# Kernel optimization log

Hardware: AMD Instinct MI355X
Metric: run time of the kernel (lower is better)

Reference implementation:

```python
import jax, jax.numpy as jnp
import numpy as np
from jax import lax

DIM = 192
HEADS = 4
HIDDEN = int(DIM * 2.66)  # 510
B, H, W = 2, 64, 64
EPS_LN = 1e-6
EPS_NORM = 1e-12


def conv1x1(x, w, b):
    # x: (b,c,h,w), w: (o,c), b: (o,)
    return jnp.einsum('bchw,oc->bohw', x, w) + b[None, :, None, None]


def dwconv3x3(x, w, b):
    # depthwise 3x3, SAME padding; w: (C,1,3,3)
    c = x.shape[1]
    y = lax.conv_general_dilated(x, w, window_strides=(1, 1), padding='SAME',
                                 feature_group_count=c,
                                 dimension_numbers=('NCHW', 'OIHW', 'NCHW'))
    return y + b[None, :, None, None]


def layernorm2d(x, w, b):
    mean = jnp.mean(x, axis=(2, 3), keepdims=True)
    var = jnp.mean((x - mean) ** 2, axis=(2, 3), keepdims=True)
    return (x - mean) / jnp.sqrt(var + EPS_LN) * w[None, :, None, None] + b[None, :, None, None]


def mdta(x, qkv_w, qkv_b, qkv_dw_w, qkv_dw_b, temperature, proj_w, proj_b):
    b, c, h, w = x.shape
    qkv = dwconv3x3(conv1x1(x, qkv_w, qkv_b), qkv_dw_w, qkv_dw_b)
    q, k, v = jnp.split(qkv, 3, axis=1)
    dh = c // HEADS
    q = q.reshape(b, HEADS, dh, h * w)
    k = k.reshape(b, HEADS, dh, h * w)
    v = v.reshape(b, HEADS, dh, h * w)
    # L2-normalize over per-head channel dim (axis=2), like F.normalize(dim=2)
    q = q / jnp.maximum(jnp.linalg.norm(q, axis=2, keepdims=True), EPS_NORM)
    k = k / jnp.maximum(jnp.linalg.norm(k, axis=2, keepdims=True), EPS_NORM)
    # spatial attention map: (b, heads, HW, HW)
    attn = jnp.einsum('bhcn,bhcm->bhnm', q, k) * temperature[None]  # temp (heads,1,1)
    attn = jax.nn.softmax(attn, axis=-1)
    out = jnp.einsum('bhnm,bhcm->bhcn', attn, v)  # (b,heads,dh,HW)
    out = out.reshape(b, c, h, w)
    return conv1x1(out, proj_w, proj_b)


def gdfn(x, pin_w, pin_b, dw_w, dw_b, pout_w, pout_b):
    y = dwconv3x3(conv1x1(x, pin_w, pin_b), dw_w, dw_b)
    y1, y2 = jnp.split(y, 2, axis=1)
    y = jax.nn.gelu(y1, approximate=False) * y2
    return conv1x1(y, pout_w, pout_b)


def setup_inputs() -> dict:
    key = jax.random.key(0)
    ks = jax.random.split(key, 8)
    s = 0.02
    return {
        'x': jax.random.normal(ks[0], (B, DIM, H, W), jnp.float32),
        'ln1_w': jnp.ones((DIM,), jnp.float32),
        'ln1_b': jnp.zeros((DIM,), jnp.float32),
        'qkv_w': jax.random.normal(ks[1], (DIM * 3, DIM), jnp.float32) * s,
        'qkv_b': jnp.zeros((DIM * 3,), jnp.float32),
        'qkv_dw_w': jax.random.normal(ks[2], (DIM * 3, 1, 3, 3), jnp.float32) * s,
        'qkv_dw_b': jnp.zeros((DIM * 3,), jnp.float32),
        'temperature': jnp.ones((HEADS, 1, 1), jnp.float32),
        'proj_w': jax.random.normal(ks[3], (DIM, DIM), jnp.float32) * s,
        'proj_b': jnp.zeros((DIM,), jnp.float32),
        'ln2_w': jnp.ones((DIM,), jnp.float32),
        'ln2_b': jnp.zeros((DIM,), jnp.float32),
        'pin_w': jax.random.normal(ks[4], (HIDDEN * 2, DIM), jnp.float32) * s,
        'pin_b': jnp.zeros((HIDDEN * 2,), jnp.float32),
        'gdfn_dw_w': jax.random.normal(ks[5], (HIDDEN * 2, 1, 3, 3), jnp.float32) * s,
        'gdfn_dw_b': jnp.zeros((HIDDEN * 2,), jnp.float32),
        'pout_w': jax.random.normal(ks[6], (DIM, HIDDEN), jnp.float32) * s,
        'pout_b': jnp.zeros((DIM,), jnp.float32),
    }


def reference(x, ln1_w, ln1_b, qkv_w, qkv_b, qkv_dw_w, qkv_dw_b, temperature,
              proj_w, proj_b, ln2_w, ln2_b, pin_w, pin_b, gdfn_dw_w, gdfn_dw_b,
              pout_w, pout_b):
    x = x + mdta(layernorm2d(x, ln1_w, ln1_b), qkv_w, qkv_b, qkv_dw_w, qkv_dw_b,
                 temperature, proj_w, proj_b)
    x = x + gdfn(layernorm2d(x, ln2_w, ln2_b), pin_w, pin_b, gdfn_dw_w, gdfn_dw_b,
                 pout_w, pout_b)
    return x
```

## Files before the change

kernel.cpp:

```cpp
#include <hip/hip_runtime.h>
#include <hip/hip_bf16.h>

typedef __bf16 bf16x8 __attribute__((ext_vector_type(8)));
typedef __bf16 bf16x4 __attribute__((ext_vector_type(4)));
typedef __bf16 bf16x2 __attribute__((ext_vector_type(2)));
typedef float f32x4 __attribute__((ext_vector_type(4)));

#define HW 4096
#define DIMC 192
#define DH 48
#define HIDC 510

__global__ void wcvt4_kernel(const float* __restrict__ qkv_w, const float* __restrict__ proj_w,
                             const float* __restrict__ pin_w, const float* __restrict__ pout_w,
                             __bf16* __restrict__ wb_qkv, __bf16* __restrict__ wb_proj,
                             __bf16* __restrict__ wb_pin, __bf16* __restrict__ wb_pout) {
  int idx = blockIdx.x * 256 + threadIdx.x;
  if (idx < 110592) {
    wb_qkv[idx] = (__bf16)qkv_w[idx];
  } else if (idx < 147456) {
    int i = idx - 110592;
    wb_proj[i] = (__bf16)proj_w[i];
  } else if (idx < 343296) {
    int i = idx - 147456;
    wb_pin[i] = (__bf16)pin_w[i];
  } else if (idx < 441600) {
    int i = idx - 343296;
    int o = i >> 9, c = i & 511;
    wb_pout[i] = (c < HIDC) ? (__bf16)pout_w[o * HIDC + c] : (__bf16)0.f;
  }
}

__global__ __launch_bounds__(256) void ln_stats_kernel(const float* __restrict__ x, const float* __restrict__ w,
                                                       const float* __restrict__ b, float* __restrict__ sc,
                                                       float* __restrict__ sh) {
  int bc = blockIdx.x;
  int c = bc % DIMC;
  const float* row = x + (size_t)bc * HW;
  float s = 0.f, s2 = 0.f;
  for (int i = threadIdx.x; i < HW; i += 256) { float v = row[i]; s += v; s2 = fmaf(v, v, s2); }
  __shared__ float red[8];
  for (int off = 32; off; off >>= 1) { s += __shfl_down(s, off, 64); s2 += __shfl_down(s2, off, 64); }
  int wid = threadIdx.x >> 6;
  if ((threadIdx.x & 63) == 0) { red[wid] = s; red[4 + wid] = s2; }
  __syncthreads();
  if (threadIdx.x == 0) {
    s = red[0] + red[1] + red[2] + red[3];
    s2 = red[4] + red[5] + red[6] + red[7];
    float mean = s * (1.f / HW);
    float var = s2 * (1.f / HW) - mean * mean;
    float rstd = rsqrtf(var + 1e-6f);
    float scv = rstd * w[c];
    sc[bc] = scv;
    sh[bc] = b[c] - mean * scv;
  }
}

__global__ __launch_bounds__(256) void ln_apply_t_kernel(const float* __restrict__ x, const float* __restrict__ sc,
                                                         const float* __restrict__ sh, __bf16* __restrict__ Xt) {
  int n0 = blockIdx.x * 64, c0 = blockIdx.y * 32, b = blockIdx.z;
  int t = threadIdx.x;
  int n = t & 63, cs = c0 + (t >> 6) * 8;
  __bf16 ob[8];
#pragma unroll
  for (int cc = 0; cc < 8; ++cc) {
    int c = cs + cc;
    float v = fmaf(x[((size_t)(b * DIMC + c)) * HW + n0 + n], sc[b * DIMC + c], sh[b * DIMC + c]);
    ob[cc] = (__bf16)v;
  }
  *(bf16x8*)&Xt[((size_t)((b << 12) + n0 + n)) * DIMC + cs] = *(bf16x8*)ob;
}

__global__ __launch_bounds__(256) void gemm_kernel(const __bf16* __restrict__ A, const __bf16* __restrict__ Bt,
                                                   const float* __restrict__ bias, const float* __restrict__ res,
                                                   float* __restrict__ outf, __bf16* __restrict__ outb,
                                                   int O, int Cs, int mode) {
  __shared__ __align__(16) __bf16 Asub[64 * 72];
  __shared__ __align__(16) __bf16 Bsub[128 * 72];
  const int t = threadIdx.x;
  const int lane = t & 63, wv = t >> 6;
  const int q4 = lane >> 4, l16 = lane & 15;
  int o0 = blockIdx.y * 64;
  if (o0 + 64 > O) o0 = O - 64;
  const int ntot0 = blockIdx.x * 128;
  const int b = ntot0 >> 12;
  const int n_in_b0 = ntot0 & 4095;

  f32x4 acc[8];
#pragma unroll
  for (int nt = 0; nt < 8; ++nt) acc[nt] = (f32x4){0.f, 0.f, 0.f, 0.f};

  for (int c0 = 0; c0 < Cs; c0 += 64) {
    __syncthreads();
#pragma unroll
    for (int j = 0; j < 2; ++j) {
      int id = t + 256 * j;
      *(bf16x8*)&Asub[(id >> 3) * 72 + (id & 7) * 8] =
          *(const bf16x8*)&A[((size_t)(o0 + (id >> 3))) * Cs + c0 + (id & 7) * 8];
    }
    if (mode != 3) {
#pragma unroll
      for (int j = 0; j < 4; ++j) {
        int id = t + 256 * j;
        *(bf16x8*)&Bsub[(id >> 3) * 72 + (id & 7) * 8] =
            *(const bf16x8*)&Bt[((size_t)(ntot0 + (id >> 3))) * Cs + c0 + (id & 7) * 8];
      }
    } else {
      int cr = t >> 2, seg = t & 3;
      int cg = c0 + cr;
      __bf16 tmp[32];
      if (cg < HIDC) {
        const __bf16* gp = Bt + ((size_t)(b * HIDC + cg)) * HW + n_in_b0 + seg * 32;
#pragma unroll
        for (int j = 0; j < 4; ++j) *(bf16x8*)&tmp[8 * j] = *(const bf16x8*)&gp[8 * j];
      } else {
#pragma unroll
        for (int k = 0; k < 32; ++k) tmp[k] = (__bf16)0.f;
      }
#pragma unroll
      for (int k = 0; k < 32; ++k) Bsub[(seg * 32 + k) * 72 + cr] = tmp[k];
    }
    __syncthreads();
#pragma unroll
    for (int ks = 0; ks < 2; ++ks) {
      bf16x8 af = *(const bf16x8*)&Asub[(16 * wv + l16) * 72 + 32 * ks + 8 * q4];
#pragma unroll
      for (int nt = 0; nt < 8; ++nt) {
        bf16x8 bfr = *(const bf16x8*)&Bsub[(16 * nt + l16) * 72 + 32 * ks + 8 * q4];
        acc[nt] = __builtin_amdgcn_mfma_f32_16x16x32_bf16(af, bfr, acc[nt], 0, 0, 0);
      }
    }
  }

  float bvals[4];
#pragma unroll
  for (int r = 0; r < 4; ++r) bvals[r] = bias[o0 + 16 * wv + 4 * q4 + r];
#pragma unroll
  for (int nt = 0; nt < 8; ++nt) {
    int n_in_b = n_in_b0 + 16 * nt + l16;
#pragma unroll
    for (int r = 0; r < 4; ++r) {
      int o = o0 + 16 * wv + 4 * q4 + r;
      size_t addr = ((size_t)(b * O + o)) * HW + n_in_b;
      float v = acc[nt][r] + bvals[r];
      if (mode >= 2) { outf[addr] = v + res[addr]; }
      else if (mode == 0) { outf[addr] = v; }
      else { outb[addr] = (__bf16)v; }
    }
  }
}

__global__ __launch_bounds__(256) void dwconv_split_kernel(const __bf16* __restrict__ in, const float* __restrict__ w,
                                                           const float* __restrict__ bias,
                                                           __bf16* __restrict__ qdwb, __bf16* __restrict__ Vbf) {
  int bc = blockIdx.x;
  int b = bc / 576, ch = bc - b * 576;
  __shared__ float tile[66 * 68];
  for (int i = threadIdx.x; i < 66 * 68; i += 256) tile[i] = 0.f;
  __syncthreads();
  const __bf16* p = in + (size_t)bc * HW;
  for (int j = 0; j < 8; ++j) {
    int i = 2 * threadIdx.x + 512 * j;
    bf16x2 v = *(const bf16x2*)&p[i];
    int y = i >> 6, xx = i & 63;
    tile[(y + 1) * 68 + xx + 1] = (float)v.x;
    tile[(y + 1) * 68 + xx + 2] = (float)v.y;
  }
  __syncthreads();
  float w0 = w[ch * 9 + 0], w1 = w[ch * 9 + 1], w2 = w[ch * 9 + 2];
  float w3 = w[ch * 9 + 3], w4 = w[ch * 9 + 4], w5 = w[ch * 9 + 5];
  float w6 = w[ch * 9 + 6], w7 = w[ch * 9 + 7], w8 = w[ch * 9 + 8];
  float bb = bias[ch];
  __bf16* dst;
  if (ch < 384) dst = qdwb + ((size_t)(b * 384 + ch)) * HW;
  else {
    int c = ch - 384, h = c / DH, cc = c - h * DH;
    dst = Vbf + ((size_t)((b * 4 + h) * DH + cc)) * HW;
  }
  for (int j = 0; j < 8; ++j) {
    int i = 2 * threadIdx.x + 512 * j;
    int y = i >> 6, xx = i & 63;
    const float* tt = &tile[y * 68 + xx];
    float a = bb;
    a = fmaf(w0, tt[0], a);   a = fmaf(w1, tt[1], a);   a = fmaf(w2, tt[2], a);
    a = fmaf(w3, tt[68], a);  a = fmaf(w4, tt[69], a);  a = fmaf(w5, tt[70], a);
    a = fmaf(w6, tt[136], a); a = fmaf(w7, tt[137], a); a = fmaf(w8, tt[138], a);
    float a2 = bb;
    a2 = fmaf(w0, tt[1], a2);   a2 = fmaf(w1, tt[2], a2);   a2 = fmaf(w2, tt[3], a2);
    a2 = fmaf(w3, tt[69], a2);  a2 = fmaf(w4, tt[70], a2);  a2 = fmaf(w5, tt[71], a2);
    a2 = fmaf(w6, tt[137], a2); a2 = fmaf(w7, tt[138], a2); a2 = fmaf(w8, tt[139], a2);
    bf16x2 o = { (__bf16)a, (__bf16)a2 };
    *(bf16x2*)&dst[i] = o;
  }
}

__global__ __launch_bounds__(256) void gdfn_dw_gate_kernel(const __bf16* __restrict__ hid, const float* __restrict__ w,
                                                           const float* __restrict__ bias, __bf16* __restrict__ gate) {
  int blk = blockIdx.x;
  int b = blk / HIDC, j = blk - b * HIDC;
  __shared__ float t1[66 * 68];
  __shared__ float t2[66 * 68];
  for (int i = threadIdx.x; i < 66 * 68; i += 256) { t1[i] = 0.f; t2[i] = 0.f; }
  __syncthreads();
  const __bf16* p1 = hid + ((size_t)b * (2 * HIDC) + j) * HW;
  const __bf16* p2 = p1 + (size_t)HIDC * HW;
  for (int i = threadIdx.x; i < HW; i += 256) {
    int y = i >> 6, xx = i & 63;
    t1[(y + 1) * 68 + xx + 1] = (float)p1[i];
    t2[(y + 1) * 68 + xx + 1] = (float)p2[i];
  }
  __syncthreads();
  int c1 = j, c2 = j + HIDC;
  float a0 = w[c1*9+0], a1w = w[c1*9+1], a2w = w[c1*9+2], a3 = w[c1*9+3], a4 = w[c1*9+4],
        a5 = w[c1*9+5], a6 = w[c1*9+6], a7 = w[c1*9+7], a8 = w[c1*9+8];
  float b0 = w[c2*9+0], b1 = w[c2*9+1], b2 = w[c2*9+2], b3 = w[c2*9+3], b4 = w[c2*9+4],
        b5 = w[c2*9+5], b6 = w[c2*9+6], b7 = w[c2*9+7], b8 = w[c2*9+8];
  float bi1 = bias[c1], bi2 = bias[c2];
  __bf16* op = gate + ((size_t)b * HIDC + j) * HW;
  for (int i = threadIdx.x; i < HW; i += 256) {
    int y = i >> 6, xx = i & 63;
    const float* u = &t1[y * 68 + xx];
    const float* v = &t2[y * 68 + xx];
    float x1 = bi1;
    x1 = fmaf(a0, u[0], x1);   x1 = fmaf(a1w, u[1], x1);  x1 = fmaf(a2w, u[2], x1);
    x1 = fmaf(a3, u[68], x1);  x1 = fmaf(a4, u[69], x1);  x1 = fmaf(a5, u[70], x1);
    x1 = fmaf(a6, u[136], x1); x1 = fmaf(a7, u[137], x1); x1 = fmaf(a8, u[138], x1);
    float x2 = bi2;
    x2 = fmaf(b0, v[0], x2);   x2 = fmaf(b1, v[1], x2);   x2 = fmaf(b2, v[2], x2);
    x2 = fmaf(b3, v[68], x2);  x2 = fmaf(b4, v[69], x2);  x2 = fmaf(b5, v[70], x2);
    x2 = fmaf(b6, v[136], x2); x2 = fmaf(b7, v[137], x2); x2 = fmaf(b8, v[138], x2);
    float g = 0.5f * x1 * (1.f + erff(x1 * 0.70710678118654752f));
    op[i] = (__bf16)(g * x2);
  }
}

__global__ __launch_bounds__(256) void prep_qk_kernel(const __bf16* __restrict__ qdwb, const float* __restrict__ temp,
                                                      __bf16* __restrict__ Qbf, __bf16* __restrict__ Kbf) {
  int gid = blockIdx.x * 256 + threadIdx.x;
  int bh = gid >> 12, n = gid & 4095;
  int b = bh >> 2, h = bh & 3;
  const __bf16* qp = qdwb + ((size_t)(b * 384 + h * DH)) * HW + n;
  const __bf16* kp = qp + (size_t)192 * HW;
  float buf[DH];
  float ss = 0.f;
#pragma unroll
  for (int c = 0; c < DH; ++c) { buf[c] = (float)qp[(size_t)c * HW]; ss = fmaf(buf[c], buf[c], ss); }
  float sc = temp[h] / fmaxf(sqrtf(ss), 1e-12f);
  __bf16 ob[64];
#pragma unroll
  for (int c = 0; c < DH; ++c) ob[c] = (__bf16)(buf[c] * sc);
#pragma unroll
  for (int c = DH; c < 64; ++c) ob[c] = (__bf16)0.f;
  __bf16* qd = Qbf + (size_t)gid * 64;
#pragma unroll
  for (int ch = 0; ch < 8; ++ch) *(bf16x8*)&qd[ch * 8] = *(bf16x8*)&ob[ch * 8];

  ss = 0.f;
#pragma unroll
  for (int c = 0; c < DH; ++c) { buf[c] = (float)kp[(size_t)c * HW]; ss = fmaf(buf[c], buf[c], ss); }
  sc = 1.f / fmaxf(sqrtf(ss), 1e-12f);
#pragma unroll
  for (int c = 0; c < DH; ++c) ob[c] = (__bf16)(buf[c] * sc);
  __bf16* kd = Kbf + (size_t)gid * 64;
#pragma unroll
  for (int ch = 0; ch < 8; ++ch) *(bf16x8*)&kd[ch * 8] = *(bf16x8*)&ob[ch * 8];
}

__global__ __launch_bounds__(256) void attn_split_kernel(const __bf16* __restrict__ Qbf, const __bf16* __restrict__ Kbf,
                                                         const __bf16* __restrict__ Vbf, float* __restrict__ part) {
  __shared__ __align__(16) __bf16 Kt[64 * 72];
  __shared__ __align__(16) __bf16 Vc[48 * 72];
  __shared__ __align__(16) __bf16 Pl[64 * 72];
  const int tid = threadIdx.x;
  const int lane = tid & 63;
  const int wv = tid >> 6;
  const int q4 = lane >> 4, l16 = lane & 15;
  const int bid = blockIdx.x;
  const int chunk = bid >> 9, rest = bid & 511;
  const int bh = rest >> 6, nt = rest & 63;
  const int n0 = nt * 64;
  const __bf16* Qg = Qbf + (size_t)bh * HW * 64;
  const __bf16* Kg = Kbf + (size_t)bh * HW * 64;
  const __bf16* Vg = Vbf + (size_t)bh * DH * HW;

  bf16x8 qf[4][2];
#pragma unroll
  for (int s = 0; s < 4; ++s)
#pragma unroll
    for (int ks = 0; ks < 2; ++ks)
      qf[s][ks] = *(const bf16x8*)&Qg[((size_t)(n0 + 16 * s + l16)) * 64 + 32 * ks + 8 * q4];

  float lsub[4] = {0.f, 0.f, 0.f, 0.f};
  f32x4 oacc[3];
#pragma unroll
  for (int ct = 0; ct < 3; ++ct) oacc[ct] = (f32x4){0.f, 0.f, 0.f, 0.f};

  for (int mt = chunk * 16; mt < chunk * 16 + 16; ++mt) {
    const int m0 = mt * 64;
    __syncthreads();
#pragma unroll
    for (int j = 0; j < 2; ++j) {
      int id = tid + 256 * j;
      *(bf16x8*)&Kt[(id >> 3) * 72 + (id & 7) * 8] = *(const bf16x8*)&Kg[((size_t)(m0 + (id >> 3))) * 64 + (id & 7) * 8];
    }
    for (int i = tid; i < 384; i += 256)
      *(bf16x8*)&Vc[(i >> 3) * 72 + (i & 7) * 8] = *(const bf16x8*)&Vg[((size_t)(i >> 3)) * HW + m0 + (i & 7) * 8];
    __syncthreads();

    f32x4 sacc[4];
#pragma unroll
    for (int s = 0; s < 4; ++s) sacc[s] = (f32x4){0.f, 0.f, 0.f, 0.f};
#pragma unroll
    for (int ks = 0; ks < 2; ++ks) {
      bf16x8 af = *(const bf16x8*)&Kt[(16 * wv + l16) * 72 + 32 * ks + 8 * q4];
#pragma unroll
      for (int s = 0; s < 4; ++s)
        sacc[s] = __builtin_amdgcn_mfma_f32_16x16x32_bf16(af, qf[s][ks], sacc[s], 0, 0, 0);
    }

#pragma unroll
    for (int s = 0; s < 4; ++s) {
      float p0 = __expf(sacc[s][0]);
      float p1 = __expf(sacc[s][1]);
      float p2 = __expf(sacc[s][2]);
      float p3 = __expf(sacc[s][3]);
      lsub[s] += (p0 + p1) + (p2 + p3);
      bf16x4 pk = { (__bf16)p0, (__bf16)p1, (__bf16)p2, (__bf16)p3 };
      *(bf16x4*)&Pl[(16 * s + l16) * 72 + 16 * wv + 4 * q4] = pk;
    }
    __syncthreads();

#pragma unroll
    for (int ks = 0; ks < 2; ++ks) {
      bf16x8 pf = *(const bf16x8*)&Pl[(16 * wv + l16) * 72 + 32 * ks + 8 * q4];
#pragma unroll
      for (int ct = 0; ct < 3; ++ct) {
        bf16x8 vf = *(const bf16x8*)&Vc[(16 * ct + l16) * 72 + 32 * ks + 8 * q4];
        oacc[ct] = __builtin_amdgcn_mfma_f32_16x16x32_bf16(pf, vf, oacc[ct], 0, 0, 0);
      }
    }
  }

  __syncthreads();
  float* Lred = (float*)Kt;
#pragma unroll
  for (int s = 0; s < 4; ++s) {
    float v = lsub[s];
    v += __shfl_xor(v, 16, 64);
    v += __shfl_xor(v, 32, 64);
    if (q4 == 0) Lred[wv * 64 + 16 * s + l16] = v;
  }
  __syncthreads();
  size_t pbase = (size_t)bid * 3136;
  if (tid < 64)
    part[pbase + 3072 + tid] = Lred[tid] + Lred[64 + tid] + Lred[128 + tid] + Lred[192 + tid];
#pragma unroll
  for (int ct = 0; ct < 3; ++ct)
#pragma unroll
    for (int r = 0; r < 4; ++r) {
      int n = 16 * wv + 4 * q4 + r;
      part[pbase + (size_t)n * 48 + 16 * ct + l16] = oacc[ct][r];
    }
}

__global__ __launch_bounds__(256) void attn_merge_kernel(const float* __restrict__ part, __bf16* __restrict__ Xt) {
  const int bid = blockIdx.x;
  const int bh = bid >> 6, nt = bid & 63;
  const int b = bh >> 2, h = bh & 3;
  const int n0 = nt * 64;
  const int t = threadIdx.x;
  __shared__ float linv[64];
  if (t < 64) {
    float s = 0.f;
#pragma unroll
    for (int ch = 0; ch < 4; ++ch) s += part[((size_t)(ch * 512 + bid)) * 3136 + 3072 + t];
    linv[t] = 1.f / s;
  }
  __syncthreads();
#pragma unroll
  for (int j = 0; j < 3; ++j) {
    int id = t + 256 * j;
    int n = id / 12, cc = (id - n * 12) * 4;
    f32x4 s = (f32x4){0.f, 0.f, 0.f, 0.f};
#pragma unroll
    for (int ch = 0; ch < 4; ++ch) s += *(const f32x4*)&part[((size_t)(ch * 512 + bid)) * 3136 + (size_t)n * 48 + cc];
    float li = linv[n];
    bf16x4 ov = { (__bf16)(s.x * li), (__bf16)(s.y * li), (__bf16)(s.z * li), (__bf16)(s.w * li) };
    *(bf16x4*)&Xt[((size_t)((b << 12) + n0 + n)) * DIMC + h * DH + cc] = ov;
  }
}

extern "C" void kernel_launch(void* const* d_in, const int* in_sizes, int n_in,
                              void* d_out, int out_size, void* d_ws, size_t ws_size,
                              hipStream_t stream) {
  const float* x        = (const float*)d_in[0];
  const float* ln1_w    = (const float*)d_in[1];
  const float* ln1_b    = (const float*)d_in[2];
  const float* qkv_w    = (const float*)d_in[3];
  const float* qkv_b    = (const float*)d_in[4];
  const float* qkv_dw_w = (const float*)d_in[5];
  const float* qkv_dw_b = (const float*)d_in[6];
  const float* temperature = (const float*)d_in[7];
  const float* proj_w   = (const float*)d_in[8];
  const float* proj_b   = (const float*)d_in[9];
  const float* ln2_w    = (const float*)d_in[10];
  const float* ln2_b    = (const float*)d_in[11];
  const float* pin_w    = (const float*)d_in[12];
  const float* pin_b    = (const float*)d_in[13];
  const float* gdfn_dw_w = (const float*)d_in[14];
  const float* gdfn_dw_b = (const float*)d_in[15];
  const float* pout_w   = (const float*)d_in[16];
  const float* pout_b   = (const float*)d_in[17];
  float* out = (float*)d_out;
  float* ws = (float*)d_ws;

  __bf16* wb_qkv  = (__bf16*)(ws + 0);
  __bf16* wb_proj = (__bf16*)(ws + 55296);
  __bf16* wb_pin  = (__bf16*)(ws + 73728);
  __bf16* wb_pout = (__bf16*)(ws + 171648);
  float* sc1 = ws + 220800;
  float* sh1 = ws + 221184;
  float* sc2 = ws + 221568;
  float* sh2 = ws + 221952;
  __bf16* Xt1 = (__bf16*)(ws + 222336);
  __bf16* Xt2 = (__bf16*)(ws + 222336);
  __bf16* Qbf = (__bf16*)(ws + 222336);
  __bf16* Kbf = (__bf16*)(ws + 1270912);
  __bf16* Vbf = (__bf16*)(ws + 2319488);
  __bf16* qkvb   = (__bf16*)(ws + 3105920);
  __bf16* Xt_att = (__bf16*)(ws + 3105920);
  __bf16* hid    = (__bf16*)(ws + 3105920);
  __bf16* qdwb  = (__bf16*)(ws + 5465216);
  float*  Opart = ws + 5465216;
  __bf16* gate  = (__bf16*)(ws + 7283840);

  wcvt4_kernel<<<1725, 256, 0, stream>>>(qkv_w, proj_w, pin_w, pout_w, wb_qkv, wb_proj, wb_pin, wb_pout);

  ln_stats_kernel<<<2 * DIMC, 256, 0, stream>>>(x, ln1_w, ln1_b, sc1, sh1);
  ln_apply_t_kernel<<<dim3(64, 6, 2), 256, 0, stream>>>(x, sc1, sh1, Xt1);
  gemm_kernel<<<dim3(64, 9), 256, 0, stream>>>(wb_qkv, Xt1, qkv_b, nullptr, nullptr, qkvb, 576, 192, 1);
  dwconv_split_kernel<<<1152, 256, 0, stream>>>(qkvb, qkv_dw_w, qkv_dw_b, qdwb, Vbf);
  prep_qk_kernel<<<128, 256, 0, stream>>>(qdwb, temperature, Qbf, Kbf);
  attn_split_kernel<<<2048, 256, 0, stream>>>(Qbf, Kbf, Vbf, Opart);
  attn_merge_kernel<<<512, 256, 0, stream>>>(Opart, Xt_att);
  gemm_kernel<<<dim3(64, 3), 256, 0, stream>>>(wb_proj, Xt_att, proj_b, x, out, nullptr, 192, 192, 2);

  ln_stats_kernel<<<2 * DIMC, 256, 0, stream>>>(out, ln2_w, ln2_b, sc2, sh2);
  ln_apply_t_kernel<<<dim3(64, 6, 2), 256, 0, stream>>>(out, sc2, sh2, Xt2);
  gemm_kernel<<<dim3(64, 16), 256, 0, stream>>>(wb_pin, Xt2, pin_b, nullptr, nullptr, hid, 1020, 192, 1);
  gdfn_dw_gate_kernel<<<2 * HIDC, 256, 0, stream>>>(hid, gdfn_dw_w, gdfn_dw_b, gate);
  gemm_kernel<<<dim3(64, 3), 256, 0, stream>>>(wb_pout, (const __bf16*)gate, pout_b, out, out, nullptr, 192, 512, 3);
}
```

Baseline: 268.9 us.

## Feed softmax probabilities straight from registers into fp16 PV MFMA

The P tile no longer round-trips through shared memory. The exponentiated scores are packed to fp16 in registers and used directly as the B operand of a 16x16x16 f16 MFMA, with V stored as fp16 so the layouts match. Each wave now holds partial O for all 64 query rows over its own 16 keys, so a cross-wave shared-memory reduction is added at the end. Q is prescaled by log2(e) so exp2f can replace __expf, and launch bounds request 4 blocks per SM. The trade is one fewer barrier and less LDS traffic per key tile, against more accumulator registers (48 floats) and an extra reduction epilogue.

```diff
diff --git a/kernel.cpp b/kernel.cpp
--- a/kernel.cpp
+++ b/kernel.cpp
@@ -4,12 +4,18 @@
 typedef __bf16 bf16x8 __attribute__((ext_vector_type(8)));
 typedef __bf16 bf16x4 __attribute__((ext_vector_type(4)));
 typedef __bf16 bf16x2 __attribute__((ext_vector_type(2)));
+typedef _Float16 f16x8 __attribute__((ext_vector_type(8)));
+typedef _Float16 f16x4 __attribute__((ext_vector_type(4)));
+typedef _Float16 f16x2 __attribute__((ext_vector_type(2)));
 typedef float f32x4 __attribute__((ext_vector_type(4)));
+
+#define MFMA16x16x16F16(a, b, c) __builtin_amdgcn_mfma_f32_16x16x16f16((a), (b), (c), 0, 0, 0)
 
 #define HW 4096
 #define DIMC 192
 #define DH 48
 #define HIDC 510
+#define LOG2E 1.44269504088896f
 
 __global__ void wcvt4_kernel(const float* __restrict__ qkv_w, const float* __restrict__ proj_w,
                              const float* __restrict__ pin_w, const float* __restrict__ pout_w,
@@ -152,7 +158,7 @@
 
 __global__ __launch_bounds__(256) void dwconv_split_kernel(const __bf16* __restrict__ in, const float* __restrict__ w,
                                                            const float* __restrict__ bias,
-                                                           __bf16* __restrict__ qdwb, __bf16* __restrict__ Vbf) {
+                                                           __bf16* __restrict__ qdwb, _Float16* __restrict__ Vh) {
   int bc = blockIdx.x;
   int b = bc / 576, ch = bc - b * 576;
   __shared__ float tile[66 * 68];
@@ -171,11 +177,12 @@
   float w3 = w[ch * 9 + 3], w4 = w[ch * 9 + 4], w5 = w[ch * 9 + 5];
   float w6 = w[ch * 9 + 6], w7 = w[ch * 9 + 7], w8 = w[ch * 9 + 8];
   float bb = bias[ch];
-  __bf16* dst;
-  if (ch < 384) dst = qdwb + ((size_t)(b * 384 + ch)) * HW;
+  const bool isv = (ch >= 384);
+  __bf16* dstq = nullptr; _Float16* dstv = nullptr;
+  if (!isv) dstq = qdwb + ((size_t)(b * 384 + ch)) * HW;
   else {
     int c = ch - 384, h = c / DH, cc = c - h * DH;
-    dst = Vbf + ((size_t)((b * 4 + h) * DH + cc)) * HW;
+    dstv = Vh + ((size_t)((b * 4 + h) * DH + cc)) * HW;
   }
   for (int j = 0; j < 8; ++j) {
     int i = 2 * threadIdx.x + 512 * j;
@@ -189,8 +196,13 @@
     a2 = fmaf(w0, tt[1], a2);   a2 = fmaf(w1, tt[2], a2);   a2 = fmaf(w2, tt[3], a2);
     a2 = fmaf(w3, tt[69], a2);  a2 = fmaf(w4, tt[70], a2);  a2 = fmaf(w5, tt[71], a2);
     a2 = fmaf(w6, tt[137], a2); a2 = fmaf(w7, tt[138], a2); a2 = fmaf(w8, tt[139], a2);
-    bf16x2 o = { (__bf16)a, (__bf16)a2 };
-    *(bf16x2*)&dst[i] = o;
+    if (!isv) {
+      bf16x2 o = { (__bf16)a, (__bf16)a2 };
+      *(bf16x2*)&dstq[i] = o;
+    } else {
+      f16x2 o = { (_Float16)a, (_Float16)a2 };
+      *(f16x2*)&dstv[i] = o;
+    }
   }
 }
 
@@ -245,7 +257,7 @@
   float ss = 0.f;
 #pragma unroll
   for (int c = 0; c < DH; ++c) { buf[c] = (float)qp[(size_t)c * HW]; ss = fmaf(buf[c], buf[c], ss); }
-  float sc = temp[h] / fmaxf(sqrtf(ss), 1e-12f);
+  float sc = temp[h] * LOG2E / fmaxf(sqrtf(ss), 1e-12f);
   __bf16 ob[64];
 #pragma unroll
   for (int c = 0; c < DH; ++c) ob[c] = (__bf16)(buf[c] * sc);
@@ -266,11 +278,12 @@
   for (int ch = 0; ch < 8; ++ch) *(bf16x8*)&kd[ch * 8] = *(bf16x8*)&ob[ch * 8];
 }
 
-__global__ __launch_bounds__(256) void attn_split_kernel(const __bf16* __restrict__ Qbf, const __bf16* __restrict__ Kbf,
-                                                         const __bf16* __restrict__ Vbf, float* __restrict__ part) {
-  __shared__ __align__(16) __bf16 Kt[64 * 72];
-  __shared__ __align__(16) __bf16 Vc[48 * 72];
-  __shared__ __align__(16) __bf16 Pl[64 * 72];
+__global__ __launch_bounds__(256, 4) void attn_split_kernel(const __bf16* __restrict__ Qbf, const __bf16* __restrict__ Kbf,
+                                                            const _Float16* __restrict__ Vh, float* __restrict__ part) {
+  __shared__ __align__(16) char smem[16384];
+  __bf16* Kt = (__bf16*)smem;
+  _Float16* Vc = (_Float16*)(smem + 9216);
+  float* sred = (float*)smem;
   const int tid = threadIdx.x;
   const int lane = tid & 63;
   const int wv = tid >> 6;
@@ -281,7 +294,7 @@
   const int n0 = nt * 64;
   const __bf16* Qg = Qbf + (size_t)bh * HW * 64;
   const __bf16* Kg = Kbf + (size_t)bh * HW * 64;
-  const __bf16* Vg = Vbf + (size_t)bh * DH * HW;
+  const _Float16* Vg = Vh + (size_t)bh * DH * HW;
 
   bf16x8 qf[4][2];
 #pragma unroll
@@ -291,9 +304,11 @@
       qf[s][ks] = *(const bf16x8*)&Qg[((size_t)(n0 + 16 * s + l16)) * 64 + 32 * ks + 8 * q4];
 
   float lsub[4] = {0.f, 0.f, 0.f, 0.f};
-  f32x4 oacc[3];
-#pragma unroll
-  for (int ct = 0; ct < 3; ++ct) oacc[ct] = (f32x4){0.f, 0.f, 0.f, 0.f};
+  f32x4 oacc[4][3];
+#pragma unroll
+  for (int s = 0; s < 4; ++s)
+#pragma unroll
+    for (int ct = 0; ct < 3; ++ct) oacc[s][ct] = (f32x4){0.f, 0.f, 0.f, 0.f};
 
   for (int mt = chunk * 16; mt < chunk * 16 + 16; ++mt) {
     const int m0 = mt * 64;
@@ -304,8 +319,13 @@
       *(bf16x8*)&Kt[(id >> 3) * 72 + (id & 7) * 8] = *(const bf16x8*)&Kg[((size_t)(m0 + (id >> 3))) * 64 + (id & 7) * 8];
     }
     for (int i = tid; i < 384; i += 256)
-      *(bf16x8*)&Vc[(i >> 3) * 72 + (i & 7) * 8] = *(const bf16x8*)&Vg[((size_t)(i >> 3)) * HW + m0 + (i & 7) * 8];
+      *(f16x8*)&Vc[(i >> 3) * 72 + (i & 7) * 8] = *(const f16x8*)&Vg[((size_t)(i >> 3)) * HW + m0 + (i & 7) * 8];
     __syncthreads();
+
+    f16x4 va[3];
+#pragma unroll
+    for (int ct = 0; ct < 3; ++ct)
+      va[ct] = *(const f16x4*)&Vc[(16 * ct + l16) * 72 + 16 * wv + 4 * q4];
 
     f32x4 sacc[4];
 #pragma unroll
@@ -320,47 +340,57 @@
 
 #pragma unroll
     for (int s = 0; s < 4; ++s) {
-      float p0 = __expf(sacc[s][0]);
-      float p1 = __expf(sacc[s][1]);
-      float p2 = __expf(sacc[s][2]);
-      float p3 = __expf(sacc[s][3]);
+      float p0 = exp2f(sacc[s][0]);
+      float p1 = exp2f(sacc[s][1]);
+      float p2 = exp2f(sacc[s][2]);
+      float p3 = exp2f(sacc[s][3]);
       lsub[s] += (p0 + p1) + (p2 + p3);
-      bf16x4 pk = { (__bf16)p0, (__bf16)p1, (__bf16)p2, (__bf16)p3 };
-      *(bf16x4*)&Pl[(16 * s + l16) * 72 + 16 * wv + 4 * q4] = pk;
-    }
-    __syncthreads();
-
-#pragma unroll
-    for (int ks = 0; ks < 2; ++ks) {
-      bf16x8 pf = *(const bf16x8*)&Pl[(16 * wv + l16) * 72 + 32 * ks + 8 * q4];
-#pragma unroll
-      for (int ct = 0; ct < 3; ++ct) {
-        bf16x8 vf = *(const bf16x8*)&Vc[(16 * ct + l16) * 72 + 32 * ks + 8 * q4];
-        oacc[ct] = __builtin_amdgcn_mfma_f32_16x16x32_bf16(pf, vf, oacc[ct], 0, 0, 0);
-      }
-    }
-  }
-
-  __syncthreads();
-  float* Lred = (float*)Kt;
+      f16x4 pk = { (_Float16)p0, (_Float16)p1, (_Float16)p2, (_Float16)p3 };
+#pragma unroll
+      for (int ct = 0; ct < 3; ++ct)
+        oacc[s][ct] = MFMA16x16x16F16(va[ct], pk, oacc[s][ct]);
+    }
+  }
+
+  __syncthreads();
+#define DUMP()  { _Pragma("unroll") for (int s = 0; s < 4; ++s) _Pragma("unroll") for (int ct = 0; ct < 3; ++ct) _Pragma("unroll") for (int r = 0; r < 4; ++r) sred[(((s * 3 + ct) * 4) + r) * 64 + (q4 << 4) + l16] = oacc[s][ct][r]; }
+#define ACCUM() { _Pragma("unroll") for (int s = 0; s < 4; ++s) _Pragma("unroll") for (int ct = 0; ct < 3; ++ct) _Pragma("unroll") for (int r = 0; r < 4; ++r) oacc[s][ct][r] += sred[(((s * 3 + ct) * 4) + r) * 64 + (q4 << 4) + l16]; }
+  if (wv == 1) DUMP();
+  __syncthreads();
+  if (wv == 0) ACCUM();
+  __syncthreads();
+  if (wv == 3) DUMP();
+  __syncthreads();
+  if (wv == 2) ACCUM();
+  __syncthreads();
+  if (wv == 2) DUMP();
+  __syncthreads();
+  if (wv == 0) ACCUM();
+  __syncthreads();
+  if (wv == 0) DUMP();
+  __syncthreads();
+  size_t pbase = (size_t)bid * 3136;
+#pragma unroll
+  for (int k2 = 0; k2 < 3; ++k2) {
+    int id = tid + 256 * k2;
+    int n = id / 12, c0 = (id - n * 12) * 4;
+    int s = n >> 4, lx = n & 15, ct = c0 >> 4, qx = (c0 >> 2) & 3;
+    f32x4 v;
+#pragma unroll
+    for (int r = 0; r < 4; ++r) v[r] = sred[((s * 3 + ct) * 4 + r) * 64 + (qx << 4) + lx];
+    *(f32x4*)&part[pbase + 4 * id] = v;
+  }
+  __syncthreads();
 #pragma unroll
   for (int s = 0; s < 4; ++s) {
     float v = lsub[s];
     v += __shfl_xor(v, 16, 64);
     v += __shfl_xor(v, 32, 64);
-    if (q4 == 0) Lred[wv * 64 + 16 * s + l16] = v;
-  }
-  __syncthreads();
-  size_t pbase = (size_t)bid * 3136;
+    if (q4 == 0) sred[wv * 64 + 16 * s + l16] = v;
+  }
+  __syncthreads();
   if (tid < 64)
-    part[pbase + 3072 + tid] = Lred[tid] + Lred[64 + tid] + Lred[128 + tid] + Lred[192 + tid];
-#pragma unroll
-  for (int ct = 0; ct < 3; ++ct)
-#pragma unroll
-    for (int r = 0; r < 4; ++r) {
-      int n = 16 * wv + 4 * q4 + r;
-      part[pbase + (size_t)n * 48 + 16 * ct + l16] = oacc[ct][r];
-    }
+    part[pbase + 3072 + tid] = sred[tid] + sred[64 + tid] + sred[128 + tid] + sred[192 + tid];
 }
 
 __global__ __launch_bounds__(256) void attn_merge_kernel(const float* __restrict__ part, __bf16* __restrict__ Xt) {
@@ -426,7 +456,7 @@
   __bf16* Xt2 = (__bf16*)(ws + 222336);
   __bf16* Qbf = (__bf16*)(ws + 222336);
   __bf16* Kbf = (__bf16*)(ws + 1270912);
-  __bf16* Vbf = (__bf16*)(ws + 2319488);
+  _Float16* Vh = (_Float16*)(ws + 2319488);
   __bf16* qkvb   = (__bf16*)(ws + 3105920);
   __bf16* Xt_att = (__bf16*)(ws + 3105920);
   __bf16* hid    = (__bf16*)(ws + 3105920);
@@ -439,9 +469,9 @@
   ln_stats_kernel<<<2 * DIMC, 256, 0, stream>>>(x, ln1_w, ln1_b, sc1, sh1);
   ln_apply_t_kernel<<<dim3(64, 6, 2), 256, 0, stream>>>(x, sc1, sh1, Xt1);
   gemm_kernel<<<dim3(64, 9), 256, 0, stream>>>(wb_qkv, Xt1, qkv_b, nullptr, nullptr, qkvb, 576, 192, 1);
-  dwconv_split_kernel<<<1152, 256, 0, stream>>>(qkvb, qkv_dw_w, qkv_dw_b, qdwb, Vbf);
+  dwconv_split_kernel<<<1152, 256, 0, stream>>>(qkvb, qkv_dw_w, qkv_dw_b, qdwb, Vh);
   prep_qk_kernel<<<128, 256, 0, stream>>>(qdwb, temperature, Qbf, Kbf);
-  attn_split_kernel<<<2048, 256, 0, stream>>>(Qbf, Kbf, Vbf, Opart);
+  attn_split_kernel<<<2048, 256, 0, stream>>>(Qbf, Kbf, Vh, Opart);
   attn_merge_kernel<<<512, 256, 0, stream>>>(Opart, Xt_att);
   gemm_kernel<<<dim3(64, 3), 256, 0, stream>>>(wb_proj, Xt_att, proj_b, x, out, nullptr, 192, 192, 2);
 
```

Result: no change. 274.1 us (+1.9%).

## Prefetch K/V tiles into registers, halve attention split, fold log2e into Q

Applied to the files above, without the earlier changes.

The attention kernel now loads the next K and V tiles into registers while the current tile is computed, so global load latency overlaps with the MFMA work. The split over keys drops from 4 chunks to 2, which halves the partial-result writes and the merge reads but also halves the number of blocks. log2(e) is folded into the Q scale so the softmax can use exp2f. The cost is extra registers per thread and lower block-level parallelism.

```diff
diff --git a/kernel.cpp b/kernel.cpp
--- a/kernel.cpp
+++ b/kernel.cpp
@@ -10,6 +10,7 @@
 #define DIMC 192
 #define DH 48
 #define HIDC 510
+#define LOG2E 1.44269504088896f
 
 __global__ void wcvt4_kernel(const float* __restrict__ qkv_w, const float* __restrict__ proj_w,
                              const float* __restrict__ pin_w, const float* __restrict__ pout_w,
@@ -245,7 +246,7 @@
   float ss = 0.f;
 #pragma unroll
   for (int c = 0; c < DH; ++c) { buf[c] = (float)qp[(size_t)c * HW]; ss = fmaf(buf[c], buf[c], ss); }
-  float sc = temp[h] / fmaxf(sqrtf(ss), 1e-12f);
+  float sc = temp[h] * LOG2E / fmaxf(sqrtf(ss), 1e-12f);
   __bf16 ob[64];
 #pragma unroll
   for (int c = 0; c < DH; ++c) ob[c] = (__bf16)(buf[c] * sc);
@@ -290,21 +291,52 @@
     for (int ks = 0; ks < 2; ++ks)
       qf[s][ks] = *(const bf16x8*)&Qg[((size_t)(n0 + 16 * s + l16)) * 64 + 32 * ks + 8 * q4];
 
+  bf16x8 kreg[2], vreg[2];
+  {
+    const int m0 = chunk * 32 * 64;
+#pragma unroll
+    for (int j = 0; j < 2; ++j) {
+      int id = tid + 256 * j;
+      kreg[j] = *(const bf16x8*)&Kg[((size_t)(m0 + (id >> 3))) * 64 + (id & 7) * 8];
+    }
+    vreg[0] = *(const bf16x8*)&Vg[((size_t)(tid >> 3)) * HW + m0 + (tid & 7) * 8];
+    if (tid < 128) {
+      int i = tid + 256;
+      vreg[1] = *(const bf16x8*)&Vg[((size_t)(i >> 3)) * HW + m0 + (i & 7) * 8];
+    }
+  }
+
   float lsub[4] = {0.f, 0.f, 0.f, 0.f};
   f32x4 oacc[3];
 #pragma unroll
   for (int ct = 0; ct < 3; ++ct) oacc[ct] = (f32x4){0.f, 0.f, 0.f, 0.f};
 
-  for (int mt = chunk * 16; mt < chunk * 16 + 16; ++mt) {
-    const int m0 = mt * 64;
+  const int mt_end = chunk * 32 + 32;
+  for (int mt = chunk * 32; mt < mt_end; ++mt) {
     __syncthreads();
 #pragma unroll
     for (int j = 0; j < 2; ++j) {
       int id = tid + 256 * j;
-      *(bf16x8*)&Kt[(id >> 3) * 72 + (id & 7) * 8] = *(const bf16x8*)&Kg[((size_t)(m0 + (id >> 3))) * 64 + (id & 7) * 8];
-    }
-    for (int i = tid; i < 384; i += 256)
-      *(bf16x8*)&Vc[(i >> 3) * 72 + (i & 7) * 8] = *(const bf16x8*)&Vg[((size_t)(i >> 3)) * HW + m0 + (i & 7) * 8];
+      *(bf16x8*)&Kt[(id >> 3) * 72 + (id & 7) * 8] = kreg[j];
+    }
+    *(bf16x8*)&Vc[(tid >> 3) * 72 + (tid & 7) * 8] = vreg[0];
+    if (tid < 128) {
+      int i = tid + 256;
+      *(bf16x8*)&Vc[(i >> 3) * 72 + (i & 7) * 8] = vreg[1];
+    }
+    if (mt + 1 < mt_end) {
+      const int m1 = (mt + 1) * 64;
+#pragma unroll
+      for (int j = 0; j < 2; ++j) {
+        int id = tid + 256 * j;
+        kreg[j] = *(const bf16x8*)&Kg[((size_t)(m1 + (id >> 3))) * 64 + (id & 7) * 8];
+      }
+      vreg[0] = *(const bf16x8*)&Vg[((size_t)(tid >> 3)) * HW + m1 + (tid & 7) * 8];
+      if (tid < 128) {
+        int i = tid + 256;
+        vreg[1] = *(const bf16x8*)&Vg[((size_t)(i >> 3)) * HW + m1 + (i & 7) * 8];
+      }
+    }
     __syncthreads();
 
     f32x4 sacc[4];
@@ -320,10 +352,10 @@
 
 #pragma unroll
     for (int s = 0; s < 4; ++s) {
-      float p0 = __expf(sacc[s][0]);
-      float p1 = __expf(sacc[s][1]);
-      float p2 = __expf(sacc[s][2]);
-      float p3 = __expf(sacc[s][3]);
+      float p0 = exp2f(sacc[s][0]);
+      float p1 = exp2f(sacc[s][1]);
+      float p2 = exp2f(sacc[s][2]);
+      float p3 = exp2f(sacc[s][3]);
       lsub[s] += (p0 + p1) + (p2 + p3);
       bf16x4 pk = { (__bf16)p0, (__bf16)p1, (__bf16)p2, (__bf16)p3 };
       *(bf16x4*)&Pl[(16 * s + l16) * 72 + 16 * wv + 4 * q4] = pk;
@@ -373,7 +405,7 @@
   if (t < 64) {
     float s = 0.f;
 #pragma unroll
-    for (int ch = 0; ch < 4; ++ch) s += part[((size_t)(ch * 512 + bid)) * 3136 + 3072 + t];
+    for (int ch = 0; ch < 2; ++ch) s += part[((size_t)(ch * 512 + bid)) * 3136 + 3072 + t];
     linv[t] = 1.f / s;
   }
   __syncthreads();
@@ -383,7 +415,7 @@
     int n = id / 12, cc = (id - n * 12) * 4;
     f32x4 s = (f32x4){0.f, 0.f, 0.f, 0.f};
 #pragma unroll
-    for (int ch = 0; ch < 4; ++ch) s += *(const f32x4*)&part[((size_t)(ch * 512 + bid)) * 3136 + (size_t)n * 48 + cc];
+    for (int ch = 0; ch < 2; ++ch) s += *(const f32x4*)&part[((size_t)(ch * 512 + bid)) * 3136 + (size_t)n * 48 + cc];
     float li = linv[n];
     bf16x4 ov = { (__bf16)(s.x * li), (__bf16)(s.y * li), (__bf16)(s.z * li), (__bf16)(s.w * li) };
     *(bf16x4*)&Xt[((size_t)((b << 12) + n0 + n)) * DIMC + h * DH + cc] = ov;
@@ -441,7 +473,7 @@
   gemm_kernel<<<dim3(64, 9), 256, 0, stream>>>(wb_qkv, Xt1, qkv_b, nullptr, nullptr, qkvb, 576, 192, 1);
   dwconv_split_kernel<<<1152, 256, 0, stream>>>(qkvb, qkv_dw_w, qkv_dw_b, qdwb, Vbf);
   prep_qk_kernel<<<128, 256, 0, stream>>>(qdwb, temperature, Qbf, Kbf);
-  attn_split_kernel<<<2048, 256, 0, stream>>>(Qbf, Kbf, Vbf, Opart);
+  attn_split_kernel<<<1024, 256, 0, stream>>>(Qbf, Kbf, Vbf, Opart);
   attn_merge_kernel<<<512, 256, 0, stream>>>(Opart, Xt_att);
   gemm_kernel<<<dim3(64, 3), 256, 0, stream>>>(wb_proj, Xt_att, proj_b, x, out, nullptr, 192, 192, 2);
 
```

Result: no change. 265.0 us (-1.5%).

## Load K and V fragments directly to registers with K prefetch, use exp2

Applied to the files above, without the earlier changes.

The attention split kernel stops staging K and V tiles through shared memory. Each wave now loads its MFMA fragments straight from global memory into registers and prefetches the next K tile while the current one is processed. This removes one barrier per iteration and cuts LDS use. The log2(e) factor is folded into the Q scaling so exp2f can replace __expf. In exchange, V reads from global are redundant across the four waves and use short strided accesses, and register pressure goes up.

```diff
diff --git a/kernel.cpp b/kernel.cpp
--- a/kernel.cpp
+++ b/kernel.cpp
@@ -10,6 +10,7 @@
 #define DIMC 192
 #define DH 48
 #define HIDC 510
+#define LOG2E 1.44269504088896f
 
 __global__ void wcvt4_kernel(const float* __restrict__ qkv_w, const float* __restrict__ proj_w,
                              const float* __restrict__ pin_w, const float* __restrict__ pout_w,
@@ -245,7 +246,7 @@
   float ss = 0.f;
 #pragma unroll
   for (int c = 0; c < DH; ++c) { buf[c] = (float)qp[(size_t)c * HW]; ss = fmaf(buf[c], buf[c], ss); }
-  float sc = temp[h] / fmaxf(sqrtf(ss), 1e-12f);
+  float sc = temp[h] * LOG2E / fmaxf(sqrtf(ss), 1e-12f);
   __bf16 ob[64];
 #pragma unroll
   for (int c = 0; c < DH; ++c) ob[c] = (__bf16)(buf[c] * sc);
@@ -268,8 +269,6 @@
 
 __global__ __launch_bounds__(256) void attn_split_kernel(const __bf16* __restrict__ Qbf, const __bf16* __restrict__ Kbf,
                                                          const __bf16* __restrict__ Vbf, float* __restrict__ part) {
-  __shared__ __align__(16) __bf16 Kt[64 * 72];
-  __shared__ __align__(16) __bf16 Vc[48 * 72];
   __shared__ __align__(16) __bf16 Pl[64 * 72];
   const int tid = threadIdx.x;
   const int lane = tid & 63;
@@ -295,54 +294,67 @@
 #pragma unroll
   for (int ct = 0; ct < 3; ++ct) oacc[ct] = (f32x4){0.f, 0.f, 0.f, 0.f};
 
-  for (int mt = chunk * 16; mt < chunk * 16 + 16; ++mt) {
+  const int mt0 = chunk * 16, mt_end = mt0 + 16;
+  bf16x8 af[2], afn[2];
+#pragma unroll
+  for (int ks = 0; ks < 2; ++ks)
+    af[ks] = *(const bf16x8*)&Kg[((size_t)(mt0 * 64 + 16 * wv + l16)) * 64 + 32 * ks + 8 * q4];
+
+  for (int mt = mt0; mt < mt_end; ++mt) {
     const int m0 = mt * 64;
+    bf16x8 vf[3][2];
+#pragma unroll
+    for (int ct = 0; ct < 3; ++ct)
+#pragma unroll
+      for (int ks = 0; ks < 2; ++ks)
+        vf[ct][ks] = *(const bf16x8*)&Vg[((size_t)(16 * ct + l16)) * HW + m0 + 32 * ks + 8 * q4];
+
+    f32x4 sacc[4];
+#pragma unroll
+    for (int s = 0; s < 4; ++s) sacc[s] = (f32x4){0.f, 0.f, 0.f, 0.f};
+#pragma unroll
+    for (int ks = 0; ks < 2; ++ks)
+#pragma unroll
+      for (int s = 0; s < 4; ++s)
+        sacc[s] = __builtin_amdgcn_mfma_f32_16x16x32_bf16(af[ks], qf[s][ks], sacc[s], 0, 0, 0);
+
+    if (mt + 1 < mt_end) {
+#pragma unroll
+      for (int ks = 0; ks < 2; ++ks)
+        afn[ks] = *(const bf16x8*)&Kg[((size_t)((mt + 1) * 64 + 16 * wv + l16)) * 64 + 32 * ks + 8 * q4];
+    }
+
+    bf16x4 pk[4];
+#pragma unroll
+    for (int s = 0; s < 4; ++s) {
+      float p0 = exp2f(sacc[s][0]);
+      float p1 = exp2f(sacc[s][1]);
+      float p2 = exp2f(sacc[s][2]);
+      float p3 = exp2f(sacc[s][3]);
+      lsub[s] += (p0 + p1) + (p2 + p3);
+      pk[s] = (bf16x4){ (__bf16)p0, (__bf16)p1, (__bf16)p2, (__bf16)p3 };
+    }
+
     __syncthreads();
 #pragma unroll
-    for (int j = 0; j < 2; ++j) {
-      int id = tid + 256 * j;
-      *(bf16x8*)&Kt[(id >> 3) * 72 + (id & 7) * 8] = *(const bf16x8*)&Kg[((size_t)(m0 + (id >> 3))) * 64 + (id & 7) * 8];
-    }
-    for (int i = tid; i < 384; i += 256)
-      *(bf16x8*)&Vc[(i >> 3) * 72 + (i & 7) * 8] = *(const bf16x8*)&Vg[((size_t)(i >> 3)) * HW + m0 + (i & 7) * 8];
-    __syncthreads();
-
-    f32x4 sacc[4];
-#pragma unroll
-    for (int s = 0; s < 4; ++s) sacc[s] = (f32x4){0.f, 0.f, 0.f, 0.f};
-#pragma unroll
-    for (int ks = 0; ks < 2; ++ks) {
-      bf16x8 af = *(const bf16x8*)&Kt[(16 * wv + l16) * 72 + 32 * ks + 8 * q4];
-#pragma unroll
-      for (int s = 0; s < 4; ++s)
-        sacc[s] = __builtin_amdgcn_mfma_f32_16x16x32_bf16(af, qf[s][ks], sacc[s], 0, 0, 0);
-    }
-
-#pragma unroll
-    for (int s = 0; s < 4; ++s) {
-      float p0 = __expf(sacc[s][0]);
-      float p1 = __expf(sacc[s][1]);
-      float p2 = __expf(sacc[s][2]);
-      float p3 = __expf(sacc[s][3]);
-      lsub[s] += (p0 + p1) + (p2 + p3);
-      bf16x4 pk = { (__bf16)p0, (__bf16)p1, (__bf16)p2, (__bf16)p3 };
-      *(bf16x4*)&Pl[(16 * s + l16) * 72 + 16 * wv + 4 * q4] = pk;
-    }
+    for (int s = 0; s < 4; ++s)
+      *(bf16x4*)&Pl[(16 * s + l16) * 72 + 16 * wv + 4 * q4] = pk[s];
     __syncthreads();
 
 #pragma unroll
     for (int ks = 0; ks < 2; ++ks) {
       bf16x8 pf = *(const bf16x8*)&Pl[(16 * wv + l16) * 72 + 32 * ks + 8 * q4];
 #pragma unroll
-      for (int ct = 0; ct < 3; ++ct) {
-        bf16x8 vf = *(const bf16x8*)&Vc[(16 * ct + l16) * 72 + 32 * ks + 8 * q4];
-        oacc[ct] = __builtin_amdgcn_mfma_f32_16x16x32_bf16(pf, vf, oacc[ct], 0, 0, 0);
-      }
-    }
-  }
-
-  __syncthreads();
-  float* Lred = (float*)Kt;
+      for (int ct = 0; ct < 3; ++ct)
+        oacc[ct] = __builtin_amdgcn_mfma_f32_16x16x32_bf16(pf, vf[ct][ks], oacc[ct], 0, 0, 0);
+    }
+
+    af[0] = afn[0];
+    af[1] = afn[1];
+  }
+
+  __syncthreads();
+  float* Lred = (float*)Pl;
 #pragma unroll
   for (int s = 0; s < 4; ++s) {
     float v = lsub[s];
```

New measurement: 329.0 us. 22.4% more time.
